# Kernel optimization log

Hardware: AMD Instinct MI355X
Metric: run time of the kernel (lower is better)

## Reference

```python
import jax, jax.numpy as jnp
import numpy as np


def setup_inputs() -> dict:
    key = jax.random.key(0)
    ks = jax.random.split(key, 8)
    B, T, D, H = 4, 4096, 1024, 64
    scale = D ** -0.5
    return {
        "x": jax.random.normal(ks[0], (B, T, D), dtype=jnp.float32),
        "mask": jax.random.randint(ks[1], (B, T), 0, 2, dtype=jnp.int32),
        "wq": jax.random.normal(ks[2], (H, D), dtype=jnp.float32) * scale,
        "bq": jax.random.normal(ks[3], (H,), dtype=jnp.float32) * 0.02,
        "wk": jax.random.normal(ks[4], (H, D), dtype=jnp.float32) * scale,
        "bk": jax.random.normal(ks[5], (H,), dtype=jnp.float32) * 0.02,
        "wv": jax.random.normal(ks[6], (H, D), dtype=jnp.float32) * scale,
        "bv": jax.random.normal(ks[7], (H,), dtype=jnp.float32) * 0.02,
    }


def reference(x, mask, wq, bq, wk, bk, wv, bv):
    # x: [B,T,D]; wq/wk/wv: [H,D] (torch Linear convention), mask: [B,T] int
    head_size = wq.shape[0]
    q = jnp.einsum("btd,hd->bth", x, wq) + bq  # [B,T,H]
    k = jnp.einsum("btd,hd->bth", x, wk) + bk
    v = jnp.einsum("btd,hd->bth", x, wv) + bv
    attn = jnp.einsum("bth,bsh->bts", q, k) * (head_size ** -0.5)  # [B,T,T]
    pad_mask = mask.astype(bool)[:, None, :]  # [B,1,T], True = keep
    attn = jnp.where(pad_mask, attn, jnp.float32(-1e9))
    attn = jax.nn.softmax(attn, axis=-1)
    # dropout is identity in eval/deterministic mode
    return jnp.einsum("bts,bsh->bth", attn, v)  # [B,T,H]
```

## Files before the change

kernel.cpp:

```cpp
#include <hip/hip_runtime.h>
#include <math.h>

#define BATCH 4
#define SEQ   4096
#define DIM   1024
#define HEAD  64
#define MROWS (BATCH*SEQ)
#define KT    64
#define QBLK  64

typedef __attribute__((ext_vector_type(8))) short short8;
typedef __attribute__((ext_vector_type(4))) float f32x4;

static __device__ __forceinline__ unsigned short f2b(float f) {
    union { float f; unsigned u; } v; v.f = f;
    return (unsigned short)((v.u + 0x7FFFu + ((v.u >> 16) & 1u)) >> 16);
}
static __device__ __forceinline__ unsigned cvtpk(float a, float b) {
    unsigned r;
    asm("v_cvt_pk_bf16_f32 %0, %1, %2" : "=v"(r) : "v"(a), "v"(b));
    return r;
}

#define QSC (0.125f * 1.4426950408889634f)
__global__ __launch_bounds__(256) void wconv_kernel(
    const float* __restrict__ wq, const float* __restrict__ bq,
    const float* __restrict__ wk, const float* __restrict__ bk,
    const float* __restrict__ wv, const float* __restrict__ bv,
    unsigned short* __restrict__ Wb, float* __restrict__ biasAll)
{
    int idx = blockIdx.x * 256 + threadIdx.x;
    int e   = idx * 4;
    int row = e >> 10;
    int col = e & 1023;
    const float* src = (row < 64) ? wq : (row < 128) ? wk : wv;
    float s = (row < 64) ? QSC : 1.0f;
    float4 g = *(const float4*)&src[(size_t)(row & 63) * DIM + col];
    ushort4 o;
    o.x = f2b(g.x * s); o.y = f2b(g.y * s); o.z = f2b(g.z * s); o.w = f2b(g.w * s);
    *(ushort4*)&Wb[e] = o;
    if (idx < 192) {
        const float* bs = (idx < 64) ? bq : (idx < 128) ? bk : bv;
        biasAll[idx] = bs[idx & 63] * ((idx < 64) ? QSC : 1.0f);
    }
}

#define NIT (DIM / 32)
__global__ __launch_bounds__(256) void qkvmm_kernel(
    const float* __restrict__ x, const unsigned short* __restrict__ Wb,
    const float* __restrict__ biasAll,
    unsigned short* __restrict__ qout, unsigned short* __restrict__ kout,
    unsigned short* __restrict__ vtout)
{
    __shared__ unsigned short xs[2][32 * 32];
    __shared__ unsigned short ws[2][192 * 32];

    const int tid  = threadIdx.x;
    const int m0   = blockIdx.x * 32;
    const int bb   = m0 >> 12;
    const int lane = tid & 63;
    const int w    = tid >> 6;
    const int lr   = lane & 15;
    const int lg   = lane >> 4;
    const int mrow  = (w >> 1) * 16;
    const int nbase = (w & 1) * 6;

    const int sxrow = tid >> 2, sxlg = tid & 3;
    int wn[3], wlg[3];
    #pragma unroll
    for (int i = 0; i < 3; ++i) { int idx = tid + i * 256; wn[i] = idx >> 2; wlg[i] = idx & 3; }

    f32x4 acc[6];
    #pragma unroll
    for (int nt = 0; nt < 6; ++nt) acc[nt] = (f32x4){0.f, 0.f, 0.f, 0.f};

    float4 xg0, xg1;
    short8 wg[3];

    auto LOADR = [&](int ko) {
        if (tid < 128) {
            const float* xp = &x[(size_t)(m0 + sxrow) * DIM + ko + sxlg * 8];
            xg0 = *(const float4*)xp;
            xg1 = *(const float4*)(xp + 4);
        }
        #pragma unroll
        for (int i = 0; i < 3; ++i)
            wg[i] = *(const short8*)&Wb[(size_t)wn[i] * DIM + ko + wlg[i] * 8];
    };
    auto WRITE = [&](int buf) {
        if (tid < 128) {
            uint4 c;
            c.x = cvtpk(xg0.x, xg0.y); c.y = cvtpk(xg0.z, xg0.w);
            c.z = cvtpk(xg1.x, xg1.y); c.w = cvtpk(xg1.z, xg1.w);
            *(uint4*)&xs[buf][sxrow * 32 + ((sxlg * 8) ^ ((sxrow & 3) * 8))] = c;
        }
        #pragma unroll
        for (int i = 0; i < 3; ++i)
            *(short8*)&ws[buf][wn[i] * 32 + ((wlg[i] * 8) ^ ((wn[i] & 3) * 8))] = wg[i];
    };

    LOADR(0);
    WRITE(0);
    __syncthreads();

    for (int it = 0; it < NIT; ++it) {
        if (it + 1 < NIT) LOADR((it + 1) * 32);
        const int cur = it & 1;
        const int arow = mrow + lr;
        short8 af = *(const short8*)&xs[cur][arow * 32 + ((lg * 8) ^ ((arow & 3) * 8))];
        #pragma unroll
        for (int nt = 0; nt < 6; ++nt) {
            int n = (nbase + nt) * 16 + lr;
            short8 bf = *(const short8*)&ws[cur][n * 32 + ((lg * 8) ^ ((n & 3) * 8))];
            acc[nt] = __builtin_amdgcn_mfma_f32_16x16x32_bf16(af, bf, acc[nt], 0, 0, 0);
        }
        if (it + 1 < NIT) WRITE((it + 1) & 1);
        __syncthreads();
    }

    #pragma unroll
    for (int nt = 0; nt < 6; ++nt) {
        int gn = (nbase + nt) * 16 + lr;
        float bv_ = biasAll[gn];
        #pragma unroll
        for (int r = 0; r < 4; ++r) {
            int grow = m0 + mrow + lg * 4 + r;
            unsigned short val = f2b(acc[nt][r] + bv_);
            if (gn < 64)       qout[(size_t)grow * HEAD + gn] = val;
            else if (gn < 128) kout[(size_t)grow * HEAD + gn - 64] = val;
            else {
                int t = (m0 & 4095) + mrow + lg * 4 + r;
                vtout[((size_t)bb * HEAD + gn - 128) * SEQ + t] = val;
            }
        }
    }
}

__global__ __launch_bounds__(256, 4) void flashmm_kernel(
    const unsigned short* __restrict__ qb, const unsigned short* __restrict__ kb,
    const unsigned short* __restrict__ vt, const int* __restrict__ mask,
    float* __restrict__ opart, float* __restrict__ mpart, float* __restrict__ lpart,
    int nsplit)
{
    const int b  = blockIdx.y;
    const int t0 = blockIdx.x * QBLK;
    const int z  = blockIdx.z;
    const int tid  = threadIdx.x;
    const int lane = tid & 63;
    const int w    = tid >> 6;
    const int lr = lane & 15;
    const int lg = lane >> 4;
    const int span = SEQ / nsplit;
    const int s_begin = z * span, s_end = s_begin + span;

    __shared__ unsigned short ks_l[KT * HEAD];
    __shared__ unsigned short vt_l[HEAD * KT];
    __shared__ unsigned short ps_l[4][16 * KT];
    __shared__ float mkf[KT];

    const unsigned short* qrow = qb + ((size_t)(b * SEQ + t0 + w * 16 + lr)) * HEAD;
    const short8 qf0 = *(const short8*)(qrow + lg * 8);
    const short8 qf1 = *(const short8*)(qrow + 32 + lg * 8);

    f32x4 acc_o[4];
    #pragma unroll
    for (int nt = 0; nt < 4; ++nt) acc_o[nt] = (f32x4){0.f, 0.f, 0.f, 0.f};
    float m_r = -INFINITY, l_r = 0.f;

    short8 kg[2], vg[2];
    float mgf = 0.f;

    auto LOADR = [&](int st) {
        #pragma unroll
        for (int i = 0; i < 2; ++i) {
            int c   = tid + i * 256;
            int row = c >> 3;
            int h0  = (c & 7) * 8;
            kg[i] = *(const short8*)(kb + ((size_t)(b * SEQ + st + row)) * HEAD + h0);
            vg[i] = *(const short8*)(vt + ((size_t)(b * HEAD + row)) * SEQ + st + h0);
        }
        if (tid < KT) mgf = (mask[(size_t)b * SEQ + st + tid] != 0) ? 0.f : -1e9f;
    };
    auto WRITE = [&]() {
        #pragma unroll
        for (int i = 0; i < 2; ++i) {
            int c   = tid + i * 256;
            int row = c >> 3;
            int h0  = (c & 7) * 8;
            *(short8*)&ks_l[row * HEAD + (h0 ^ ((row & 7) << 3))] = kg[i];
            *(short8*)&vt_l[row * KT + (h0 ^ ((row & 7) << 3))] = vg[i];
        }
        if (tid < KT) mkf[tid] = mgf;
    };

    LOADR(s_begin);
    for (int st = s_begin; st < s_end; st += KT) {
        __syncthreads();
        WRITE();
        __syncthreads();
        if (st + KT < s_end) LOADR(st + KT);

        f32x4 sT[4];
        __builtin_amdgcn_s_setprio(1);
        #pragma unroll
        for (int ct = 0; ct < 4; ++ct) {
            int krow = ct * 16 + lr;
            short8 kf0 = *(const short8*)&ks_l[krow * HEAD + ((lg * 8) ^ ((krow & 7) << 3))];
            short8 kf1 = *(const short8*)&ks_l[krow * HEAD + ((32 + lg * 8) ^ ((krow & 7) << 3))];
            f32x4 zz = (f32x4){0.f, 0.f, 0.f, 0.f};
            zz = __builtin_amdgcn_mfma_f32_16x16x32_bf16(kf0, qf0, zz, 0, 0, 0);
            zz = __builtin_amdgcn_mfma_f32_16x16x32_bf16(kf1, qf1, zz, 0, 0, 0);
            sT[ct] = zz;
        }
        __builtin_amdgcn_s_setprio(0);

        #pragma unroll
        for (int ct = 0; ct < 4; ++ct) {
            f32x4 mb = *(const f32x4*)&mkf[ct * 16 + lg * 4];
            sT[ct][0] += mb[0]; sT[ct][1] += mb[1];
            sT[ct][2] += mb[2]; sT[ct][3] += mb[3];
        }

        float mx = sT[0][0];
        #pragma unroll
        for (int ct = 0; ct < 4; ++ct)
            #pragma unroll
            for (int r = 0; r < 4; ++r) mx = fmaxf(mx, sT[ct][r]);
        mx = fmaxf(mx, __shfl_xor(mx, 16));
        mx = fmaxf(mx, __shfl_xor(mx, 32));

        bool defer = __all(mx <= m_r + 8.f);
        float base = defer ? m_r : fmaxf(m_r, mx);

        float rs = 0.f;
        #pragma unroll
        for (int ct = 0; ct < 4; ++ct)
            #pragma unroll
            for (int r = 0; r < 4; ++r) {
                float p = __builtin_amdgcn_exp2f(sT[ct][r] - base);
                sT[ct][r] = p;
                rs += p;
            }
        rs += __shfl_xor(rs, 16);
        rs += __shfl_xor(rs, 32);

        if (defer) {
            l_r += rs;
        } else {
            float sf = __builtin_amdgcn_exp2f(m_r - base);
            l_r = l_r * sf + rs;
            m_r = base;
            #pragma unroll
            for (int r = 0; r < 4; ++r) {
                float sfr = __shfl(sf, lg * 4 + r);
                #pragma unroll
                for (int nt = 0; nt < 4; ++nt) acc_o[nt][r] *= sfr;
            }
        }

        #pragma unroll
        for (int ct = 0; ct < 4; ++ct) {
            uint2 pk;
            pk.x = cvtpk(sT[ct][0], sT[ct][1]);
            pk.y = cvtpk(sT[ct][2], sT[ct][3]);
            *(uint2*)&ps_l[w][lr * KT + ((ct * 16 + lg * 4) ^ ((lr & 7) << 3))] = pk;
        }

        __builtin_amdgcn_s_setprio(1);
        #pragma unroll
        for (int kk = 0; kk < 2; ++kk) {
            int s0 = kk * 32 + lg * 8;
            short8 pf = *(const short8*)&ps_l[w][lr * KT + (s0 ^ ((lr & 7) << 3))];
            #pragma unroll
            for (int nt = 0; nt < 4; ++nt) {
                int hrow = nt * 16 + lr;
                short8 vf = *(const short8*)&vt_l[hrow * KT + (s0 ^ ((hrow & 7) << 3))];
                acc_o[nt] = __builtin_amdgcn_mfma_f32_16x16x32_bf16(pf, vf, acc_o[nt], 0, 0, 0);
            }
        }
        __builtin_amdgcn_s_setprio(0);
    }

    const size_t rbase = (size_t)z * MROWS + (size_t)b * SEQ + t0 + w * 16;
    const size_t obase = rbase * HEAD;
    #pragma unroll
    for (int nt = 0; nt < 4; ++nt)
        #pragma unroll
        for (int r = 0; r < 4; ++r) {
            int R = lg * 4 + r;
            opart[obase + (size_t)R * HEAD + nt * 16 + lr] = acc_o[nt][r];
        }
    if (lg == 0) {
        mpart[rbase + lr] = m_r;
        lpart[rbase + lr] = l_r;
    }
}

__global__ __launch_bounds__(256) void combine_kernel(
    const float* __restrict__ op, const float* __restrict__ mp,
    const float* __restrict__ lp, float* __restrict__ out, int nsplit)
{
    int idx = blockIdx.x * 256 + threadIdx.x;
    int row = idx >> 4;
    int h4  = (idx & 15) * 4;
    float mstar = -INFINITY;
    for (int s = 0; s < nsplit; ++s)
        mstar = fmaxf(mstar, mp[(size_t)s * MROWS + row]);
    float L = 0.f;
    float ax = 0.f, ay = 0.f, az = 0.f, aw = 0.f;
    for (int s = 0; s < nsplit; ++s) {
        float wgt = __builtin_amdgcn_exp2f(mp[(size_t)s * MROWS + row] - mstar);
        L += lp[(size_t)s * MROWS + row] * wgt;
        float4 o = *(const float4*)&op[((size_t)s * MROWS + row) * HEAD + h4];
        ax += o.x * wgt; ay += o.y * wgt; az += o.z * wgt; aw += o.w * wgt;
    }
    float r = 1.f / L;
    float4 res; res.x = ax * r; res.y = ay * r; res.z = az * r; res.w = aw * r;
    *(float4*)&out[(size_t)row * HEAD + h4] = res;
}

extern "C" void kernel_launch(void* const* d_in, const int* in_sizes, int n_in,
                              void* d_out, int out_size, void* d_ws, size_t ws_size,
                              hipStream_t stream) {
    const float* x    = (const float*)d_in[0];
    const int*   mask = (const int*)d_in[1];
    const float* wq   = (const float*)d_in[2];
    const float* bq   = (const float*)d_in[3];
    const float* wk   = (const float*)d_in[4];
    const float* bk   = (const float*)d_in[5];
    const float* wv   = (const float*)d_in[6];
    const float* bv   = (const float*)d_in[7];
    float* out = (float*)d_out;
    (void)in_sizes; (void)n_in; (void)out_size;

    const size_t NB = (size_t)MROWS * HEAD;
    unsigned short* qw  = (unsigned short*)d_ws;
    unsigned short* kw  = qw + NB;
    unsigned short* vtw = kw + NB;
    unsigned short* Wb  = vtw + NB;
    float* biasAll = (float*)(Wb + (size_t)192 * DIM);
    float* mpart   = biasAll + 192;

    const size_t base = 3 * NB * 2 + (size_t)192 * DIM * 2 + 192 * 4;
    const size_t per  = (size_t)MROWS * 8 + NB * 4;
    int KS = 1;
    if      (ws_size >= base + 8 * per) KS = 8;
    else if (ws_size >= base + 4 * per) KS = 4;
    else if (ws_size >= base + 2 * per) KS = 2;

    float* lpart = mpart + (size_t)KS * MROWS;
    float* opart = lpart + (size_t)KS * MROWS;

    wconv_kernel<<<dim3(192), 256, 0, stream>>>(wq, bq, wk, bk, wv, bv, Wb, biasAll);
    qkvmm_kernel<<<dim3(MROWS / 32), 256, 0, stream>>>(x, Wb, biasAll, qw, kw, vtw);
    flashmm_kernel<<<dim3(SEQ / QBLK, BATCH, KS), 256, 0, stream>>>(qw, kw, vtw, mask,
                                                                    opart, mpart, lpart, KS);
    combine_kernel<<<dim3(MROWS * 16 / 256), 256, 0, stream>>>(opart, mpart, lpart, out, KS);
}
```

Before: 80.41 us.

## Widen QKV GEMM K-tile to 64, pad weight rows, cap split-K at 4

The QKV projection GEMM now uses a 64-wide K tile in a single LDS buffer. It drops the double-buffered 32-wide scheme, keeps the register prefetch of the next tile, and uses an 8-way XOR swizzle. Weight rows are padded to 1040 elements to avoid global-memory channel aliasing, and the MFMA section runs at raised wave priority with a 4-waves-per-EU launch bound. The flash-attention split-K factor is capped at 4 instead of 8, which reduces partial-result traffic in the combine step but also reduces grid parallelism. Moving to one LDS buffer adds an extra barrier per iteration.

```diff
diff --git a/kernel.cpp b/kernel.cpp
--- a/kernel.cpp
+++ b/kernel.cpp
@@ -6,8 +6,12 @@
 #define DIM   1024
 #define HEAD  64
 #define MROWS (BATCH*SEQ)
+#define NCOL  192
+#define WST   1040
 #define KT    64
 #define QBLK  64
+#define BK2   64
+#define NIT2  (DIM / BK2)
 
 typedef __attribute__((ext_vector_type(8))) short short8;
 typedef __attribute__((ext_vector_type(4))) float f32x4;
@@ -38,22 +42,21 @@
     float4 g = *(const float4*)&src[(size_t)(row & 63) * DIM + col];
     ushort4 o;
     o.x = f2b(g.x * s); o.y = f2b(g.y * s); o.z = f2b(g.z * s); o.w = f2b(g.w * s);
-    *(ushort4*)&Wb[e] = o;
+    *(ushort4*)&Wb[(size_t)row * WST + col] = o;
     if (idx < 192) {
         const float* bs = (idx < 64) ? bq : (idx < 128) ? bk : bv;
         biasAll[idx] = bs[idx & 63] * ((idx < 64) ? QSC : 1.0f);
     }
 }
 
-#define NIT (DIM / 32)
-__global__ __launch_bounds__(256) void qkvmm_kernel(
+__global__ __launch_bounds__(256, 4) void qkvmm_kernel(
     const float* __restrict__ x, const unsigned short* __restrict__ Wb,
     const float* __restrict__ biasAll,
     unsigned short* __restrict__ qout, unsigned short* __restrict__ kout,
     unsigned short* __restrict__ vtout)
 {
-    __shared__ unsigned short xs[2][32 * 32];
-    __shared__ unsigned short ws[2][192 * 32];
+    __shared__ unsigned short xs[32 * BK2];
+    __shared__ unsigned short ws[NCOL * BK2];
 
     const int tid  = threadIdx.x;
     const int m0   = blockIdx.x * 32;
@@ -65,57 +68,63 @@
     const int mrow  = (w >> 1) * 16;
     const int nbase = (w & 1) * 6;
 
-    const int sxrow = tid >> 2, sxlg = tid & 3;
-    int wn[3], wlg[3];
-    #pragma unroll
-    for (int i = 0; i < 3; ++i) { int idx = tid + i * 256; wn[i] = idx >> 2; wlg[i] = idx & 3; }
+    int wrow[6], wc[6];
+    #pragma unroll
+    for (int j = 0; j < 6; ++j) { int L = j * 256 + tid; wrow[j] = L >> 3; wc[j] = L & 7; }
+    const int xr = tid >> 2, xq = tid & 3;
 
     f32x4 acc[6];
     #pragma unroll
     for (int nt = 0; nt < 6; ++nt) acc[nt] = (f32x4){0.f, 0.f, 0.f, 0.f};
 
-    float4 xg0, xg1;
-    short8 wg[3];
+    float4 xg[4];
+    short8 wg[6];
 
     auto LOADR = [&](int ko) {
         if (tid < 128) {
-            const float* xp = &x[(size_t)(m0 + sxrow) * DIM + ko + sxlg * 8];
-            xg0 = *(const float4*)xp;
-            xg1 = *(const float4*)(xp + 4);
-        }
-        #pragma unroll
-        for (int i = 0; i < 3; ++i)
-            wg[i] = *(const short8*)&Wb[(size_t)wn[i] * DIM + ko + wlg[i] * 8];
+            const float* xp = &x[(size_t)(m0 + xr) * DIM + ko + xq * 16];
+            xg[0] = *(const float4*)xp;       xg[1] = *(const float4*)(xp + 4);
+            xg[2] = *(const float4*)(xp + 8); xg[3] = *(const float4*)(xp + 12);
+        }
+        #pragma unroll
+        for (int j = 0; j < 6; ++j)
+            wg[j] = *(const short8*)&Wb[(size_t)wrow[j] * WST + ko + wc[j] * 8];
     };
-    auto WRITE = [&](int buf) {
+    auto WRITE = [&]() {
         if (tid < 128) {
-            uint4 c;
-            c.x = cvtpk(xg0.x, xg0.y); c.y = cvtpk(xg0.z, xg0.w);
-            c.z = cvtpk(xg1.x, xg1.y); c.w = cvtpk(xg1.z, xg1.w);
-            *(uint4*)&xs[buf][sxrow * 32 + ((sxlg * 8) ^ ((sxrow & 3) * 8))] = c;
-        }
-        #pragma unroll
-        for (int i = 0; i < 3; ++i)
-            *(short8*)&ws[buf][wn[i] * 32 + ((wlg[i] * 8) ^ ((wn[i] & 3) * 8))] = wg[i];
+            uint4 c0, c1;
+            c0.x = cvtpk(xg[0].x, xg[0].y); c0.y = cvtpk(xg[0].z, xg[0].w);
+            c0.z = cvtpk(xg[1].x, xg[1].y); c0.w = cvtpk(xg[1].z, xg[1].w);
+            c1.x = cvtpk(xg[2].x, xg[2].y); c1.y = cvtpk(xg[2].z, xg[2].w);
+            c1.z = cvtpk(xg[3].x, xg[3].y); c1.w = cvtpk(xg[3].z, xg[3].w);
+            *(uint4*)&xs[xr * BK2 + (((2 * xq)     ^ (xr & 7)) * 8)] = c0;
+            *(uint4*)&xs[xr * BK2 + (((2 * xq + 1) ^ (xr & 7)) * 8)] = c1;
+        }
+        #pragma unroll
+        for (int j = 0; j < 6; ++j)
+            *(short8*)&ws[wrow[j] * BK2 + ((wc[j] ^ (wrow[j] & 7)) * 8)] = wg[j];
     };
 
     LOADR(0);
-    WRITE(0);
-    __syncthreads();
-
-    for (int it = 0; it < NIT; ++it) {
-        if (it + 1 < NIT) LOADR((it + 1) * 32);
-        const int cur = it & 1;
-        const int arow = mrow + lr;
-        short8 af = *(const short8*)&xs[cur][arow * 32 + ((lg * 8) ^ ((arow & 3) * 8))];
-        #pragma unroll
-        for (int nt = 0; nt < 6; ++nt) {
-            int n = (nbase + nt) * 16 + lr;
-            short8 bf = *(const short8*)&ws[cur][n * 32 + ((lg * 8) ^ ((n & 3) * 8))];
-            acc[nt] = __builtin_amdgcn_mfma_f32_16x16x32_bf16(af, bf, acc[nt], 0, 0, 0);
-        }
-        if (it + 1 < NIT) WRITE((it + 1) & 1);
+    for (int it = 0; it < NIT2; ++it) {
         __syncthreads();
+        WRITE();
+        __syncthreads();
+        if (it + 1 < NIT2) LOADR((it + 1) * BK2);
+
+        __builtin_amdgcn_s_setprio(1);
+        #pragma unroll
+        for (int h = 0; h < 2; ++h) {
+            const int arow = mrow + lr;
+            short8 af = *(const short8*)&xs[arow * BK2 + (((h * 4 + lg) ^ (arow & 7)) * 8)];
+            #pragma unroll
+            for (int nt = 0; nt < 6; ++nt) {
+                int n = (nbase + nt) * 16 + lr;
+                short8 bf = *(const short8*)&ws[n * BK2 + (((h * 4 + lg) ^ (n & 7)) * 8)];
+                acc[nt] = __builtin_amdgcn_mfma_f32_16x16x32_bf16(af, bf, acc[nt], 0, 0, 0);
+            }
+        }
+        __builtin_amdgcn_s_setprio(0);
     }
 
     #pragma unroll
@@ -338,14 +347,13 @@
     unsigned short* kw  = qw + NB;
     unsigned short* vtw = kw + NB;
     unsigned short* Wb  = vtw + NB;
-    float* biasAll = (float*)(Wb + (size_t)192 * DIM);
+    float* biasAll = (float*)(Wb + (size_t)NCOL * WST);
     float* mpart   = biasAll + 192;
 
-    const size_t base = 3 * NB * 2 + (size_t)192 * DIM * 2 + 192 * 4;
+    const size_t base = 3 * NB * 2 + (size_t)NCOL * WST * 2 + 192 * 4;
     const size_t per  = (size_t)MROWS * 8 + NB * 4;
     int KS = 1;
-    if      (ws_size >= base + 8 * per) KS = 8;
-    else if (ws_size >= base + 4 * per) KS = 4;
+    if      (ws_size >= base + 4 * per) KS = 4;
     else if (ws_size >= base + 2 * per) KS = 2;
 
     float* lpart = mpart + (size_t)KS * MROWS;
```

After: 74.44 us (median of 2 runs). 7.4% less time.
